# Performance work log

Measured on AMD Instinct MI355X. Metric: run time of the kernel, lower is better.

The kernel has to match this reference:

```python
import jax, jax.numpy as jnp
import numpy as np

EPSILON = 1e-05
LOG_2PI = float(np.log(2.0 * np.pi))


def setup_inputs() -> dict:
    key = jax.random.key(0)
    k1, k2, k3 = jax.random.split(key, 3)
    B, S, K, N = 64, 1000, 12, 80  # batch, seq, n_states, n_channels
    x = jax.random.normal(k1, (B, S, N), dtype=jnp.float32)
    mu = jax.random.normal(k2, (B, K, N), dtype=jnp.float32)
    # Positive-definite covariances per (batch, state)
    A = jax.random.normal(k3, (B, K, N, N), dtype=jnp.float32)
    sigma = A @ jnp.swapaxes(A, -1, -2) / N + jnp.eye(N, dtype=jnp.float32)
    return {"x": x, "mu": mu, "sigma": sigma}


def reference(x, mu, sigma):
    """Batched-over-states MVN log-likelihood.

    x: (B, S, N); mu: (B, K, N); sigma: (B, K, N, N).
    Returns log_likelihood: (B, S, K).
    """
    N = x.shape[-1]
    # add_epsilon with diag=True: epsilon * I on the diagonal
    sigma = sigma + jnp.asarray(EPSILON, sigma.dtype) * jnp.eye(N, dtype=sigma.dtype)
    L = jnp.linalg.cholesky(sigma)  # (B, K, N, N), batched across states
    diff = x[:, :, None, :] - mu[:, None, :, :]  # (B, S, K, N)
    # Solve L z = diff, batched: L -> (B, 1, K, N, N), diff -> (B, S, K, N, 1)
    z = jax.scipy.linalg.solve_triangular(L[:, None], diff[..., None], lower=True)[..., 0]
    quad = jnp.sum(z * z, axis=-1)  # (B, S, K)
    logdet_half = jnp.sum(jnp.log(jnp.diagonal(L, axis1=-2, axis2=-1)), axis=-1)  # (B, K)
    ll = -0.5 * quad - logdet_half[:, None, :] - 0.5 * N * jnp.asarray(LOG_2PI, x.dtype)
    return ll  # (B, S, K)
```

## Files before the change

### kernel.cpp

```cpp
#include <hip/hip_runtime.h>

#define Bb 64
#define Ss 1000
#define Kk 12
#define Nn 80
#define CTERM 73.51508265637381f
#define STA 84

typedef __attribute__((ext_vector_type(8))) short short8;
typedef __attribute__((ext_vector_type(4))) float f32x4;

static __device__ __forceinline__ unsigned short f2bf(float f) {
    unsigned u = __builtin_bit_cast(unsigned, f);
    unsigned r = u + 0x7FFFu + ((u >> 16) & 1u);
    return (unsigned short)(r >> 16);
}
static __device__ __forceinline__ float bf2f(unsigned short h) {
    unsigned u = ((unsigned)h) << 16;
    return __builtin_bit_cast(float, u);
}

__global__ __launch_bounds__(512, 6) void prep_kernel(
    const float* __restrict__ sigma, const float* __restrict__ mu,
    const float* __restrict__ x,
    uint4* __restrict__ wsWh, uint4* __restrict__ wsWl,
    float* __restrict__ wsV, float* __restrict__ wsL,
    uint4* __restrict__ Xh, uint4* __restrict__ Xl, int doX)
{
    __shared__ float Ls[Nn * STA];
    __shared__ float invd[Nn];
    __shared__ float mus[Nn];
    __shared__ float ldp[8];
    __shared__ float vps[8 * Nn];

    const int bk  = blockIdx.x;
    const int tid = threadIdx.x;
    const int w   = tid >> 6;
    const int l   = tid & 63;
    const int r2  = l + 64;

    const float4* sp4 = (const float4*)(sigma + (size_t)bk * Nn * Nn);
    #pragma unroll
    for (int it = 0; it < 4; ++it) {
        int ci = tid + 512 * it;
        if (ci < 1600) {
            int r = ci / 20, c4 = 4 * (ci - 20 * r);
            if (c4 <= r + 3) {
                float4 v = sp4[ci];
                *(float4*)&Ls[r * STA + c4] = v;
            }
        }
    }
    if (tid < Nn) mus[tid] = mu[(size_t)bk * Nn + tid];
    __syncthreads();
    if (tid < Nn) Ls[tid * STA + tid] += 1e-5f;
    __syncthreads();

    float ldacc = 0.0f;
    for (int p = 0; p < 20; ++p) {
        const int j0 = 4 * p;
        const bool a1 = (l >= j0);
        const bool a2 = (l < 16) && (r2 >= j0);

        if (w == (p & 7)) {
            float B00 = Ls[j0*STA+j0];
            float B10 = Ls[(j0+1)*STA+j0], B11 = Ls[(j0+1)*STA+j0+1];
            float B20 = Ls[(j0+2)*STA+j0], B21 = Ls[(j0+2)*STA+j0+1], B22 = Ls[(j0+2)*STA+j0+2];
            float B30 = Ls[(j0+3)*STA+j0], B31 = Ls[(j0+3)*STA+j0+1], B32 = Ls[(j0+3)*STA+j0+2], B33 = Ls[(j0+3)*STA+j0+3];
            float rv0 = rsqrtf(B00);
            float l10 = B10*rv0, l20 = B20*rv0, l30 = B30*rv0;
            float t11 = fmaf(-l10,l10,B11);                    float rv1 = rsqrtf(t11);
            float l21 = fmaf(-l20,l10,B21)*rv1;
            float l31 = fmaf(-l30,l10,B31)*rv1;
            float t22 = fmaf(-l21,l21,fmaf(-l20,l20,B22));     float rv2 = rsqrtf(t22);
            float l32 = fmaf(-l31,l21,fmaf(-l30,l20,B32))*rv2;
            float t33 = fmaf(-l32,l32,fmaf(-l31,l31,fmaf(-l30,l30,B33)));
            float rv3 = rsqrtf(t33);
            ldacc += 0.5f * (logf(B00) + logf(t11) + logf(t22) + logf(t33));
            if (l == 0) { invd[j0]=rv0; invd[j0+1]=rv1; invd[j0+2]=rv2; invd[j0+3]=rv3; }

            if (a1) {
                float4 a = *(float4*)&Ls[l * STA + j0];
                float b0 = a.x * rv0;
                float b1 = fmaf(-l10, b0, a.y) * rv1;
                float b2 = fmaf(-l21, b1, fmaf(-l20, b0, a.z)) * rv2;
                float b3 = fmaf(-l32, b2, fmaf(-l31, b1, fmaf(-l30, b0, a.w))) * rv3;
                *(float4*)&Ls[l * STA + j0] = make_float4(b0, b1, b2, b3);
            }
            if (a2) {
                float4 a = *(float4*)&Ls[r2 * STA + j0];
                float c0 = a.x * rv0;
                float c1 = fmaf(-l10, c0, a.y) * rv1;
                float c2 = fmaf(-l21, c1, fmaf(-l20, c0, a.z)) * rv2;
                float c3 = fmaf(-l32, c2, fmaf(-l31, c1, fmaf(-l30, c0, a.w))) * rv3;
                *(float4*)&Ls[r2 * STA + j0] = make_float4(c0, c1, c2, c3);
            }
        }
        __syncthreads();

        const int gs0 = p + 1;
        const int g0 = gs0 + ((w - gs0) & 7);
        #pragma unroll 2
        for (int g = g0; g < 20; g += 8) {
            const int cb = 4 * g;
            float4 q0 = *(const float4*)&Ls[(cb+0) * STA + j0];
            float4 q1 = *(const float4*)&Ls[(cb+1) * STA + j0];
            float4 q2 = *(const float4*)&Ls[(cb+2) * STA + j0];
            float4 q3 = *(const float4*)&Ls[(cb+3) * STA + j0];
            {
                const int R = cb + l;
                if (R < Nn) {
                    float4 pv = *(const float4*)&Ls[R * STA + j0];
                    float4 t  = *(float4*)&Ls[R * STA + cb];
                    t.x = fmaf(-pv.x,q0.x, fmaf(-pv.y,q0.y, fmaf(-pv.z,q0.z, fmaf(-pv.w,q0.w, t.x))));
                    t.y = fmaf(-pv.x,q1.x, fmaf(-pv.y,q1.y, fmaf(-pv.z,q1.z, fmaf(-pv.w,q1.w, t.y))));
                    t.z = fmaf(-pv.x,q2.x, fmaf(-pv.y,q2.y, fmaf(-pv.z,q2.z, fmaf(-pv.w,q2.w, t.z))));
                    t.w = fmaf(-pv.x,q3.x, fmaf(-pv.y,q3.y, fmaf(-pv.z,q3.z, fmaf(-pv.w,q3.w, t.w))));
                    *(float4*)&Ls[R * STA + cb] = t;
                }
            }
            if (cb + 64 < Nn) {
                const int R = cb + 64 + l;
                if (R < Nn) {
                    float4 pv = *(const float4*)&Ls[R * STA + j0];
                    float4 t  = *(float4*)&Ls[R * STA + cb];
                    t.x = fmaf(-pv.x,q0.x, fmaf(-pv.y,q0.y, fmaf(-pv.z,q0.z, fmaf(-pv.w,q0.w, t.x))));
                    t.y = fmaf(-pv.x,q1.x, fmaf(-pv.y,q1.y, fmaf(-pv.z,q1.z, fmaf(-pv.w,q1.w, t.y))));
                    t.z = fmaf(-pv.x,q2.x, fmaf(-pv.y,q2.y, fmaf(-pv.z,q2.z, fmaf(-pv.w,q2.w, t.z))));
                    t.w = fmaf(-pv.x,q3.x, fmaf(-pv.y,q3.y, fmaf(-pv.z,q3.z, fmaf(-pv.w,q3.w, t.w))));
                    *(float4*)&Ls[R * STA + cb] = t;
                }
            }
        }
    }
    if (l == 0) ldp[w] = ldacc;
    __syncthreads();
    if (tid == 0) wsL[bk] = ldp[0]+ldp[1]+ldp[2]+ldp[3]+ldp[4]+ldp[5]+ldp[6]+ldp[7];

    for (int i = tid; i < Nn * Nn; i += 512) {
        int r = i / Nn, c = i - Nn * r;
        if (c > r) Ls[r * STA + c] = 0.0f;
    }
    __syncthreads();

    for (int p = 0; p < 20; ++p) {
        const int i0 = 4 * p;
        const bool b1a = (i0 + 3 >= l);
        const bool b2a = (l < 16) && (i0 + 3 >= r2);

        if (w == (p & 7)) {
            float m10 = Ls[(i0+1)*STA + i0];
            float m20 = Ls[(i0+2)*STA + i0];
            float m30 = Ls[(i0+3)*STA + i0];
            float m21 = Ls[(i0+2)*STA + i0+1];
            float m31 = Ls[(i0+3)*STA + i0+1];
            float m32 = Ls[(i0+3)*STA + i0+2];
            float4 iv = *(const float4*)&invd[i0];
            if (b1a) {
                float4 a = *(float4*)&Ls[l * STA + i0];
                if (l >= i0)
                    a = make_float4(l==i0?1.f:0.f, l==i0+1?1.f:0.f, l==i0+2?1.f:0.f, l==i0+3?1.f:0.f);
                float w0 = a.x * iv.x;
                float w1 = fmaf(-w0, m10, a.y) * iv.y;
                float w2 = fmaf(-w1, m21, fmaf(-w0, m20, a.z)) * iv.z;
                float w3 = fmaf(-w2, m32, fmaf(-w1, m31, fmaf(-w0, m30, a.w))) * iv.w;
                *(float4*)&Ls[l * STA + i0] = make_float4(w0, w1, w2, w3);
            }
            if (b2a) {
                float4 a = *(float4*)&Ls[r2 * STA + i0];
                if (r2 >= i0)
                    a = make_float4(r2==i0?1.f:0.f, r2==i0+1?1.f:0.f, r2==i0+2?1.f:0.f, r2==i0+3?1.f:0.f);
                float v0 = a.x * iv.x;
                float v1 = fmaf(-v0, m10, a.y) * iv.y;
                float v2 = fmaf(-v1, m21, fmaf(-v0, m20, a.z)) * iv.z;
                float v3 = fmaf(-v2, m32, fmaf(-v1, m31, fmaf(-v0, m30, a.w))) * iv.w;
                *(float4*)&Ls[r2 * STA + i0] = make_float4(v0, v1, v2, v3);
            }
        }
        __syncthreads();

        float4 wv = make_float4(0.f,0.f,0.f,0.f), vv = make_float4(0.f,0.f,0.f,0.f);
        if (b1a) wv = *(float4*)&Ls[l * STA + i0];
        if (b2a) vv = *(float4*)&Ls[r2 * STA + i0];
        if (b1a | b2a) {
            const int gs0 = p + 1;
            const int g0 = gs0 + ((w - gs0) & 7);
            for (int g = g0; g < 20; g += 8) {
                float4 q0 = *(const float4*)&Ls[(4*g+0) * STA + i0];
                float4 q1 = *(const float4*)&Ls[(4*g+1) * STA + i0];
                float4 q2 = *(const float4*)&Ls[(4*g+2) * STA + i0];
                float4 q3 = *(const float4*)&Ls[(4*g+3) * STA + i0];
                if (b1a) {
                    float4 t = *(float4*)&Ls[l * STA + 4*g];
                    t.x = fmaf(-wv.x,q0.x, fmaf(-wv.y,q0.y, fmaf(-wv.z,q0.z, fmaf(-wv.w,q0.w, t.x))));
                    t.y = fmaf(-wv.x,q1.x, fmaf(-wv.y,q1.y, fmaf(-wv.z,q1.z, fmaf(-wv.w,q1.w, t.y))));
                    t.z = fmaf(-wv.x,q2.x, fmaf(-wv.y,q2.y, fmaf(-wv.z,q2.z, fmaf(-wv.w,q2.w, t.z))));
                    t.w = fmaf(-wv.x,q3.x, fmaf(-wv.y,q3.y, fmaf(-wv.z,q3.z, fmaf(-wv.w,q3.w, t.w))));
                    *(float4*)&Ls[l * STA + 4*g] = t;
                }
                if (b2a) {
                    float4 t = *(float4*)&Ls[r2 * STA + 4*g];
                    t.x = fmaf(-vv.x,q0.x, fmaf(-vv.y,q0.y, fmaf(-vv.z,q0.z, fmaf(-vv.w,q0.w, t.x))));
                    t.y = fmaf(-vv.x,q1.x, fmaf(-vv.y,q1.y, fmaf(-vv.z,q1.z, fmaf(-vv.w,q1.w, t.y))));
                    t.z = fmaf(-vv.x,q2.x, fmaf(-vv.y,q2.y, fmaf(-vv.z,q2.z, fmaf(-vv.w,q2.w, t.z))));
                    t.w = fmaf(-vv.x,q3.x, fmaf(-vv.y,q3.y, fmaf(-vv.z,q3.z, fmaf(-vv.w,q3.w, t.w))));
                    *(float4*)&Ls[r2 * STA + 4*g] = t;
                }
            }
        }
    }
    __syncthreads();

    {
        float s1 = 0.f, s2 = 0.f;
        const int c0 = 10 * w;
        #pragma unroll 2
        for (int cc = 0; cc < 10; ++cc) {
            int c = c0 + cc;
            float mc = mus[c];
            float e1 = (c <= l)  ? Ls[c * STA + l]  : 0.f;
            s1 = fmaf(e1, mc, s1);
            if (l < 16) {
                float e2 = (c <= r2) ? Ls[c * STA + r2] : 0.f;
                s2 = fmaf(e2, mc, s2);
            }
        }
        vps[w * Nn + l] = s1;
        if (l < 16) vps[w * Nn + r2] = s2;
        __syncthreads();
        if (tid < Nn) {
            float acc = 0.f;
            #pragma unroll
            for (int ww = 0; ww < 8; ++ww) acc += vps[ww * Nn + tid];
            wsV[(size_t)bk * Nn + tid] = acc;
        }
    }

    const int n = l & 15, quad = l >> 4;
    uint4* ph = wsWh + (size_t)bk * 800;
    uint4* pq = wsWl + (size_t)bk * 800;
    for (int f = w; f < 10; f += 8) {
        int ks = f / 5, mt = f - 5 * ks;
        int m = 16 * mt + n, kb = 32 * ks + 8 * quad;
        unsigned hh[8], lo[8];
        #pragma unroll
        for (int j = 0; j < 8; ++j) {
            float wj = (m >= kb + j) ? Ls[(kb + j) * STA + m] : 0.f;
            unsigned short h = f2bf(wj);
            hh[j] = h; lo[j] = f2bf(wj - bf2f(h));
        }
        ph[f*64 + l] = make_uint4(hh[0]|(hh[1]<<16), hh[2]|(hh[3]<<16), hh[4]|(hh[5]<<16), hh[6]|(hh[7]<<16));
        pq[f*64 + l] = make_uint4(lo[0]|(lo[1]<<16), lo[2]|(lo[3]<<16), lo[4]|(lo[5]<<16), lo[6]|(lo[7]<<16));
    }
    if (w < 5) {
        int mt = w;
        if (quad < 2) {
            int m = 16 * mt + n, kb = 64 + 8 * quad;
            unsigned hh[8], lo[8];
            #pragma unroll
            for (int j = 0; j < 8; ++j) {
                float wj = (m >= kb + j) ? Ls[(kb + j) * STA + m] : 0.f;
                unsigned short h = f2bf(wj);
                hh[j] = h; lo[j] = f2bf(wj - bf2f(h));
            }
            ph[640 + mt*32 + l] = make_uint4(hh[0]|(hh[1]<<16), hh[2]|(hh[3]<<16), hh[4]|(hh[5]<<16), hh[6]|(hh[7]<<16));
            pq[640 + mt*32 + l] = make_uint4(lo[0]|(lo[1]<<16), lo[2]|(lo[3]<<16), lo[4]|(lo[5]<<16), lo[6]|(lo[7]<<16));
        }
    }

    if (doX) {
        const int wid = bk * 8 + w;
        const int qd = l >> 4, n2 = l & 15;
        #pragma unroll
        for (int it = 0; it < 2; ++it) {
            int G = wid + 6144 * it;
            if (G >= 12096) break;
            int b2  = G / 189;
            int rem = G - b2 * 189;
            int sg  = rem / 3, ks = rem - 3 * sg;
            int s   = sg * 16 + n2;
            int k0  = 32 * ks + 8 * qd;
            float d[8] = {0.f,0.f,0.f,0.f,0.f,0.f,0.f,0.f};
            if (s < Ss) {
                const float* xp = x + ((size_t)b2 * Ss + s) * Nn + k0;
                float4 f0 = *(const float4*)xp;
                float4 f1 = *(const float4*)(xp + 4);
                d[0]=f0.x; d[1]=f0.y; d[2]=f0.z; d[3]=f0.w;
                d[4]=f1.x; d[5]=f1.y; d[6]=f1.z; d[7]=f1.w;
            }
            unsigned hh[8], lo[8];
            #pragma unroll
            for (int j = 0; j < 8; ++j) {
                unsigned short h = f2bf(d[j]);
                hh[j] = h; lo[j] = f2bf(d[j] - bf2f(h));
            }
            size_t slot = ((size_t)(b2 * 64 + sg) * 3 + ks) * 64 + l;
            Xh[slot] = make_uint4(hh[0]|(hh[1]<<16), hh[2]|(hh[3]<<16), hh[4]|(hh[5]<<16), hh[6]|(hh[7]<<16));
            Xl[slot] = make_uint4(lo[0]|(lo[1]<<16), lo[2]|(lo[3]<<16), lo[4]|(lo[5]<<16), lo[6]|(lo[7]<<16));
        }
    }
}

__global__ __launch_bounds__(256) void ll_kernel2(
    const uint4* __restrict__ Xh, const uint4* __restrict__ Xl,
    const uint4* __restrict__ wsWh, const uint4* __restrict__ wsWl,
    const float* __restrict__ wsV, const float* __restrict__ wsL,
    float* __restrict__ out)
{
    __shared__ uint4 WhL[960], WlL[960];
    const int b = blockIdx.x;
    const int k = blockIdx.y;
    const int bk = b * Kk + k;
    const int tid = threadIdx.x;
    const int wv = tid >> 6, lane = tid & 63;
    const int n = lane & 15, quad = lane >> 4;

    const uint4* gh = wsWh + (size_t)bk * 800;
    const uint4* gl = wsWl + (size_t)bk * 800;
    #pragma unroll
    for (int it = 0; it < 3; ++it) {
        int i = tid + 256 * it;
        if (i < 640) { WhL[i] = gh[i]; WlL[i] = gl[i]; }
    }
    #pragma unroll
    for (int it = 0; it < 2; ++it) {
        int i = tid + 256 * it;
        if (i < 320) {
            int mt = i >> 6, ln = i & 63, qd = (ln >> 4);
            uint4 vh = make_uint4(0,0,0,0), vl = make_uint4(0,0,0,0);
            if (qd < 2) { vh = gh[640 + mt*32 + ln]; vl = gl[640 + mt*32 + ln]; }
            WhL[640 + i] = vh; WlL[640 + i] = vl;
        }
    }
    __syncthreads();

    const float ld = wsL[bk];
    f32x4 vf[5];
    #pragma unroll
    for (int mt = 0; mt < 5; ++mt)
        vf[mt] = *(const f32x4*)&wsV[(size_t)bk * Nn + 16*mt + 4*quad];

    for (int st = 0; st < 8; ++st) {
        const int sg0 = st * 8 + wv * 2;
        short8 bh[2][3], bl[2][3];
        #pragma unroll
        for (int t = 0; t < 2; ++t)
            #pragma unroll
            for (int ks = 0; ks < 3; ++ks) {
                size_t base = ((size_t)(b * 64 + sg0 + t) * 3 + ks) * 64 + lane;
                bh[t][ks] = __builtin_bit_cast(short8, Xh[base]);
                bl[t][ks] = __builtin_bit_cast(short8, Xl[base]);
            }

        f32x4 acc[2][5];
        #pragma unroll
        for (int t = 0; t < 2; ++t)
            #pragma unroll
            for (int mt = 0; mt < 5; ++mt) acc[t][mt] = (f32x4){0.f,0.f,0.f,0.f};

        #pragma unroll
        for (int ks = 0; ks < 3; ++ks) {
            #pragma unroll
            for (int mt = 0; mt < 5; ++mt) {
                const int fi = (ks < 2) ? (ks*5 + mt)*64 + lane : 640 + mt*64 + lane;
                short8 wh = __builtin_bit_cast(short8, WhL[fi]);
                short8 wl = __builtin_bit_cast(short8, WlL[fi]);
                #pragma unroll
                for (int t = 0; t < 2; ++t) {
                    acc[t][mt] = __builtin_amdgcn_mfma_f32_16x16x32_bf16(wh, bh[t][ks], acc[t][mt], 0, 0, 0);
                    acc[t][mt] = __builtin_amdgcn_mfma_f32_16x16x32_bf16(wl, bh[t][ks], acc[t][mt], 0, 0, 0);
                    acc[t][mt] = __builtin_amdgcn_mfma_f32_16x16x32_bf16(wh, bl[t][ks], acc[t][mt], 0, 0, 0);
                }
            }
        }

        #pragma unroll
        for (int t = 0; t < 2; ++t) {
            float q2 = 0.f;
            #pragma unroll
            for (int mt = 0; mt < 5; ++mt)
                #pragma unroll
                for (int r = 0; r < 4; ++r) {
                    float y = acc[t][mt][r] - vf[mt][r];
                    q2 = fmaf(y, y, q2);
                }
            q2 += __shfl_xor(q2, 16, 64);
            q2 += __shfl_xor(q2, 32, 64);
            int gs = st * 128 + wv * 32 + 16 * t + n;
            if (lane < 16 && gs < Ss)
                out[((size_t)b * Ss + gs) * Kk + k] = -0.5f * q2 - ld - CTERM;
        }
    }
}

__global__ __launch_bounds__(256) void ll_kernel(
    const float* __restrict__ x,
    const uint4* __restrict__ wsWh, const uint4* __restrict__ wsWl,
    const float* __restrict__ wsV, const float* __restrict__ wsL,
    float* __restrict__ out)
{
    const int b    = blockIdx.x;
    const int st   = blockIdx.y;
    const int tid  = threadIdx.x;
    const int wv   = tid >> 6, lane = tid & 63;
    const int n    = lane & 15, quad = lane >> 4;
    const int sbase = st * 128 + wv * 32;

    short8 xh[2][3], xl[2][3];
    #pragma unroll
    for (int t = 0; t < 2; ++t) {
        int gs = sbase + 16 * t + n;
        #pragma unroll
        for (int ks = 0; ks < 3; ++ks) {
            int kb = 32 * ks + 8 * quad;
            float d[8] = {0.f,0.f,0.f,0.f,0.f,0.f,0.f,0.f};
            if (gs < Ss && kb < Nn) {
                const float* xp = x + ((size_t)b * Ss + gs) * Nn + kb;
                float4 f0 = *(const float4*)xp;
                float4 f1 = *(const float4*)(xp + 4);
                d[0]=f0.x; d[1]=f0.y; d[2]=f0.z; d[3]=f0.w;
                d[4]=f1.x; d[5]=f1.y; d[6]=f1.z; d[7]=f1.w;
            }
            short8 h, lo2;
            #pragma unroll
            for (int j = 0; j < 8; ++j) {
                unsigned short hv = f2bf(d[j]);
                h[j]   = (short)hv;
                lo2[j] = (short)f2bf(d[j] - bf2f(hv));
            }
            xh[t][ks] = h; xl[t][ks] = lo2;
        }
    }

    for (int k = 0; k < Kk; ++k) {
        const int bk = b * Kk + k;
        const uint4* ah_p = wsWh + (size_t)bk * 800;
        const uint4* al_p = wsWl + (size_t)bk * 800;

        f32x4 acc[2][5];
        #pragma unroll
        for (int t = 0; t < 2; ++t)
            #pragma unroll
            for (int mt = 0; mt < 5; ++mt) acc[t][mt] = (f32x4){0.f,0.f,0.f,0.f};

        #pragma unroll
        for (int ks = 0; ks < 3; ++ks) {
            short8 ah[5], al[5];
            if (ks < 2) {
                #pragma unroll
                for (int mt = 0; mt < 5; ++mt) {
                    ah[mt] = __builtin_bit_cast(short8, ah_p[(ks*5 + mt)*64 + lane]);
                    al[mt] = __builtin_bit_cast(short8, al_p[(ks*5 + mt)*64 + lane]);
                }
            } else {
                #pragma unroll
                for (int mt = 0; mt < 5; ++mt) {
                    uint4 zh = make_uint4(0,0,0,0), zl = make_uint4(0,0,0,0);
                    if (quad < 2) {
                        zh = ah_p[640 + mt*32 + lane];
                        zl = al_p[640 + mt*32 + lane];
                    }
                    ah[mt] = __builtin_bit_cast(short8, zh);
                    al[mt] = __builtin_bit_cast(short8, zl);
                }
            }
            #pragma unroll
            for (int mt = 0; mt < 5; ++mt)
                #pragma unroll
                for (int t = 0; t < 2; ++t) {
                    acc[t][mt] = __builtin_amdgcn_mfma_f32_16x16x32_bf16(ah[mt], xh[t][ks], acc[t][mt], 0, 0, 0);
                    acc[t][mt] = __builtin_amdgcn_mfma_f32_16x16x32_bf16(al[mt], xh[t][ks], acc[t][mt], 0, 0, 0);
                    acc[t][mt] = __builtin_amdgcn_mfma_f32_16x16x32_bf16(ah[mt], xl[t][ks], acc[t][mt], 0, 0, 0);
                }
        }

        float ld = wsL[bk];
        f32x4 vf[5];
        #pragma unroll
        for (int mt = 0; mt < 5; ++mt)
            vf[mt] = *(const f32x4*)&wsV[(size_t)bk * Nn + 16*mt + 4*quad];
        #pragma unroll
        for (int t = 0; t < 2; ++t) {
            float q2 = 0.f;
            #pragma unroll
            for (int mt = 0; mt < 5; ++mt)
                #pragma unroll
                for (int r = 0; r < 4; ++r) {
                    float y = acc[t][mt][r] - vf[mt][r];
                    q2 = fmaf(y, y, q2);
                }
            q2 += __shfl_xor(q2, 16, 64);
            q2 += __shfl_xor(q2, 32, 64);
            int gs = sbase + 16 * t + n;
            if (lane < 16 && gs < Ss)
                out[((size_t)b * Ss + gs) * Kk + k] = -0.5f * q2 - ld - CTERM;
        }
    }
}

#define ST1 81
__global__ __launch_bounds__(256) void mvn_ll_fallback(
    const float* __restrict__ x, const float* __restrict__ mu,
    const float* __restrict__ sigma, float* __restrict__ out)
{
    __shared__ float Ls[Nn * ST1];
    __shared__ float invd[Nn];
    __shared__ float mus[Nn];
    __shared__ float logdet_s;

    const int bk = blockIdx.x, b = bk / Kk, k = bk - b * Kk;
    const int tid = threadIdx.x, nt = blockDim.x;

    const float* sp = sigma + (size_t)bk * Nn * Nn;
    for (int t = tid; t < Nn * Nn; t += nt) Ls[(t / Nn) * ST1 + (t % Nn)] = sp[t];
    if (tid < Nn) mus[tid] = mu[(size_t)bk * Nn + tid];
    __syncthreads();
    if (tid < Nn) Ls[tid * ST1 + tid] += 1e-5f;
    __syncthreads();
    for (int j = 0; j < Nn; ++j) {
        if (tid == 0) {
            float d = sqrtf(Ls[j * ST1 + j]);
            Ls[j * ST1 + j] = d; invd[j] = 1.0f / d;
        }
        __syncthreads();
        const float inv = invd[j];
        for (int i = j + 1 + tid; i < Nn; i += nt) Ls[i * ST1 + j] *= inv;
        __syncthreads();
        for (int t = tid; t < Nn * Nn; t += nt) {
            int r = t / Nn, c = t % Nn;
            if (r > j && c > j && c <= r)
                Ls[r * ST1 + c] -= Ls[r * ST1 + j] * Ls[c * ST1 + j];
        }
        __syncthreads();
    }
    if (tid == 0) {
        float a = 0.f; for (int j = 0; j < Nn; ++j) a += logf(Ls[j * ST1 + j]);
        logdet_s = a;
    }
    __syncthreads();
    const float ld = logdet_s;
    for (int s = tid; s < Ss; s += nt) {
        const float4* xp = (const float4*)(x + ((size_t)b * Ss + s) * Nn);
        float a[Nn];
        #pragma unroll
        for (int q = 0; q < Nn / 4; ++q) {
            float4 v = xp[q];
            a[4*q+0] = v.x - mus[4*q+0]; a[4*q+1] = v.y - mus[4*q+1];
            a[4*q+2] = v.z - mus[4*q+2]; a[4*q+3] = v.w - mus[4*q+3];
        }
        #pragma unroll
        for (int i = 0; i < Nn; ++i) {
            float t = a[i];
            #pragma unroll
            for (int j = 0; j < i; ++j) t = fmaf(-Ls[i * ST1 + j], a[j], t);
            a[i] = t * invd[i];
        }
        float quad = 0.f;
        #pragma unroll
        for (int i = 0; i < Nn; ++i) quad = fmaf(a[i], a[i], quad);
        out[((size_t)b * Ss + s) * Kk + k] = -0.5f * quad - ld - CTERM;
    }
}

extern "C" void kernel_launch(void* const* d_in, const int* in_sizes, int n_in,
                              void* d_out, int out_size, void* d_ws, size_t ws_size,
                              hipStream_t stream) {
    const float* x     = (const float*)d_in[0];
    const float* mu    = (const float*)d_in[1];
    const float* sigma = (const float*)d_in[2];
    float* out = (float*)d_out;

    const size_t nBK   = (size_t)Bb * Kk;
    const size_t nWu4  = nBK * 800;
    const size_t nXu4  = (size_t)Bb * 64 * 3 * 64;
    const size_t need_mid  = nWu4 * 16 * 2 + nBK * Nn * 4 + nBK * 4;
    const size_t need_full = need_mid + nXu4 * 16 * 2;

    if (ws_size >= need_full) {
        uint4* wsWh = (uint4*)d_ws;
        uint4* wsWl = wsWh + nWu4;
        uint4* Xh   = wsWl + nWu4;
        uint4* Xl   = Xh + nXu4;
        float* wsV  = (float*)(Xl + nXu4);
        float* wsL  = wsV + nBK * Nn;
        prep_kernel<<<dim3(Bb * Kk), dim3(512), 0, stream>>>(
            sigma, mu, x, wsWh, wsWl, wsV, wsL, Xh, Xl, 1);
        ll_kernel2<<<dim3(Bb, Kk), dim3(256), 0, stream>>>(Xh, Xl, wsWh, wsWl, wsV, wsL, out);
    } else if (ws_size >= need_mid) {
        uint4* wsWh = (uint4*)d_ws;
        uint4* wsWl = wsWh + nWu4;
        float* wsV  = (float*)(wsWl + nWu4);
        float* wsL  = wsV + nBK * Nn;
        prep_kernel<<<dim3(Bb * Kk), dim3(512), 0, stream>>>(
            sigma, mu, x, wsWh, wsWl, wsV, wsL, (uint4*)nullptr, (uint4*)nullptr, 0);
        ll_kernel<<<dim3(Bb, 8), dim3(256), 0, stream>>>(x, wsWh, wsWl, wsV, wsL, out);
    } else {
        mvn_ll_fallback<<<dim3(Bb * Kk), dim3(256), 0, stream>>>(x, mu, sigma, out);
    }
}
```

Before: 161.6 us.

## Fuse Cholesky prep and MFMA log-likelihood into a single kernel

Merges the Cholesky/bf16-split prep kernel and the MFMA quadratic-form kernel into one kernel with one block per (batch, state). The split weights, mu-projection and log-determinant stay in shared memory instead of going through a workspace, and each block converts x to bf16 hi/lo itself. This removes a kernel launch, the workspace round trip and the separate pre-conversion of x. In exchange, x is reconverted 12 times per batch (once per state), shared memory grows with the extra weight arrays, and the fallback paths are deleted.

After: 335.4 us. 108% more time.

```diff
diff --git a/kernel.cpp b/kernel.cpp
--- a/kernel.cpp
+++ b/kernel.cpp
@@ -20,20 +20,21 @@
     return __builtin_bit_cast(float, u);
 }
 
-__global__ __launch_bounds__(512, 6) void prep_kernel(
+__global__ __launch_bounds__(512, 6) void fused_ll_kernel(
     const float* __restrict__ sigma, const float* __restrict__ mu,
-    const float* __restrict__ x,
-    uint4* __restrict__ wsWh, uint4* __restrict__ wsWl,
-    float* __restrict__ wsV, float* __restrict__ wsL,
-    uint4* __restrict__ Xh, uint4* __restrict__ Xl, int doX)
+    const float* __restrict__ x, float* __restrict__ out)
 {
     __shared__ float Ls[Nn * STA];
+    __shared__ uint4 WhL[800], WlL[800];
     __shared__ float invd[Nn];
     __shared__ float mus[Nn];
+    __shared__ float vls[Nn];
     __shared__ float ldp[8];
-    __shared__ float vps[8 * Nn];
-
-    const int bk  = blockIdx.x;
+    __shared__ float lds_ld;
+
+    const int b   = blockIdx.x;
+    const int k   = blockIdx.y;
+    const int bk  = b * Kk + k;
     const int tid = threadIdx.x;
     const int w   = tid >> 6;
     const int l   = tid & 63;
@@ -135,7 +136,7 @@
     }
     if (l == 0) ldp[w] = ldacc;
     __syncthreads();
-    if (tid == 0) wsL[bk] = ldp[0]+ldp[1]+ldp[2]+ldp[3]+ldp[4]+ldp[5]+ldp[6]+ldp[7];
+    if (tid == 0) lds_ld = ldp[0]+ldp[1]+ldp[2]+ldp[3]+ldp[4]+ldp[5]+ldp[6]+ldp[7];
 
     for (int i = tid; i < Nn * Nn; i += 512) {
         int r = i / Nn, c = i - Nn * r;
@@ -212,6 +213,7 @@
     __syncthreads();
 
     {
+        float* vps = (float*)WhL;
         float s1 = 0.f, s2 = 0.f;
         const int c0 = 10 * w;
         #pragma unroll 2
@@ -232,13 +234,12 @@
             float acc = 0.f;
             #pragma unroll
             for (int ww = 0; ww < 8; ++ww) acc += vps[ww * Nn + tid];
-            wsV[(size_t)bk * Nn + tid] = acc;
-        }
+            vls[tid] = acc;
+        }
+        __syncthreads();
     }
 
     const int n = l & 15, quad = l >> 4;
-    uint4* ph = wsWh + (size_t)bk * 800;
-    uint4* pq = wsWl + (size_t)bk * 800;
     for (int f = w; f < 10; f += 8) {
         int ks = f / 5, mt = f - 5 * ks;
         int m = 16 * mt + n, kb = 32 * ks + 8 * quad;
@@ -249,8 +250,8 @@
             unsigned short h = f2bf(wj);
             hh[j] = h; lo[j] = f2bf(wj - bf2f(h));
         }
-        ph[f*64 + l] = make_uint4(hh[0]|(hh[1]<<16), hh[2]|(hh[3]<<16), hh[4]|(hh[5]<<16), hh[6]|(hh[7]<<16));
-        pq[f*64 + l] = make_uint4(lo[0]|(lo[1]<<16), lo[2]|(lo[3]<<16), lo[4]|(lo[5]<<16), lo[6]|(lo[7]<<16));
+        WhL[f*64 + l] = make_uint4(hh[0]|(hh[1]<<16), hh[2]|(hh[3]<<16), hh[4]|(hh[5]<<16), hh[6]|(hh[7]<<16));
+        WlL[f*64 + l] = make_uint4(lo[0]|(lo[1]<<16), lo[2]|(lo[3]<<16), lo[4]|(lo[5]<<16), lo[6]|(lo[7]<<16));
     }
     if (w < 5) {
         int mt = w;
@@ -263,153 +264,18 @@
                 unsigned short h = f2bf(wj);
                 hh[j] = h; lo[j] = f2bf(wj - bf2f(h));
             }
-            ph[640 + mt*32 + l] = make_uint4(hh[0]|(hh[1]<<16), hh[2]|(hh[3]<<16), hh[4]|(hh[5]<<16), hh[6]|(hh[7]<<16));
-            pq[640 + mt*32 + l] = make_uint4(lo[0]|(lo[1]<<16), lo[2]|(lo[3]<<16), lo[4]|(lo[5]<<16), lo[6]|(lo[7]<<16));
-        }
-    }
-
-    if (doX) {
-        const int wid = bk * 8 + w;
-        const int qd = l >> 4, n2 = l & 15;
-        #pragma unroll
-        for (int it = 0; it < 2; ++it) {
-            int G = wid + 6144 * it;
-            if (G >= 12096) break;
-            int b2  = G / 189;
-            int rem = G - b2 * 189;
-            int sg  = rem / 3, ks = rem - 3 * sg;
-            int s   = sg * 16 + n2;
-            int k0  = 32 * ks + 8 * qd;
-            float d[8] = {0.f,0.f,0.f,0.f,0.f,0.f,0.f,0.f};
-            if (s < Ss) {
-                const float* xp = x + ((size_t)b2 * Ss + s) * Nn + k0;
-                float4 f0 = *(const float4*)xp;
-                float4 f1 = *(const float4*)(xp + 4);
-                d[0]=f0.x; d[1]=f0.y; d[2]=f0.z; d[3]=f0.w;
-                d[4]=f1.x; d[5]=f1.y; d[6]=f1.z; d[7]=f1.w;
-            }
-            unsigned hh[8], lo[8];
-            #pragma unroll
-            for (int j = 0; j < 8; ++j) {
-                unsigned short h = f2bf(d[j]);
-                hh[j] = h; lo[j] = f2bf(d[j] - bf2f(h));
-            }
-            size_t slot = ((size_t)(b2 * 64 + sg) * 3 + ks) * 64 + l;
-            Xh[slot] = make_uint4(hh[0]|(hh[1]<<16), hh[2]|(hh[3]<<16), hh[4]|(hh[5]<<16), hh[6]|(hh[7]<<16));
-            Xl[slot] = make_uint4(lo[0]|(lo[1]<<16), lo[2]|(lo[3]<<16), lo[4]|(lo[5]<<16), lo[6]|(lo[7]<<16));
-        }
-    }
-}
-
-__global__ __launch_bounds__(256) void ll_kernel2(
-    const uint4* __restrict__ Xh, const uint4* __restrict__ Xl,
-    const uint4* __restrict__ wsWh, const uint4* __restrict__ wsWl,
-    const float* __restrict__ wsV, const float* __restrict__ wsL,
-    float* __restrict__ out)
-{
-    __shared__ uint4 WhL[960], WlL[960];
-    const int b = blockIdx.x;
-    const int k = blockIdx.y;
-    const int bk = b * Kk + k;
-    const int tid = threadIdx.x;
-    const int wv = tid >> 6, lane = tid & 63;
-    const int n = lane & 15, quad = lane >> 4;
-
-    const uint4* gh = wsWh + (size_t)bk * 800;
-    const uint4* gl = wsWl + (size_t)bk * 800;
-    #pragma unroll
-    for (int it = 0; it < 3; ++it) {
-        int i = tid + 256 * it;
-        if (i < 640) { WhL[i] = gh[i]; WlL[i] = gl[i]; }
-    }
-    #pragma unroll
-    for (int it = 0; it < 2; ++it) {
-        int i = tid + 256 * it;
-        if (i < 320) {
-            int mt = i >> 6, ln = i & 63, qd = (ln >> 4);
-            uint4 vh = make_uint4(0,0,0,0), vl = make_uint4(0,0,0,0);
-            if (qd < 2) { vh = gh[640 + mt*32 + ln]; vl = gl[640 + mt*32 + ln]; }
-            WhL[640 + i] = vh; WlL[640 + i] = vl;
-        }
-    }
-    __syncthreads();
-
-    const float ld = wsL[bk];
-    f32x4 vf[5];
-    #pragma unroll
-    for (int mt = 0; mt < 5; ++mt)
-        vf[mt] = *(const f32x4*)&wsV[(size_t)bk * Nn + 16*mt + 4*quad];
-
-    for (int st = 0; st < 8; ++st) {
-        const int sg0 = st * 8 + wv * 2;
-        short8 bh[2][3], bl[2][3];
-        #pragma unroll
-        for (int t = 0; t < 2; ++t)
-            #pragma unroll
-            for (int ks = 0; ks < 3; ++ks) {
-                size_t base = ((size_t)(b * 64 + sg0 + t) * 3 + ks) * 64 + lane;
-                bh[t][ks] = __builtin_bit_cast(short8, Xh[base]);
-                bl[t][ks] = __builtin_bit_cast(short8, Xl[base]);
-            }
-
-        f32x4 acc[2][5];
-        #pragma unroll
-        for (int t = 0; t < 2; ++t)
-            #pragma unroll
-            for (int mt = 0; mt < 5; ++mt) acc[t][mt] = (f32x4){0.f,0.f,0.f,0.f};
-
-        #pragma unroll
-        for (int ks = 0; ks < 3; ++ks) {
-            #pragma unroll
-            for (int mt = 0; mt < 5; ++mt) {
-                const int fi = (ks < 2) ? (ks*5 + mt)*64 + lane : 640 + mt*64 + lane;
-                short8 wh = __builtin_bit_cast(short8, WhL[fi]);
-                short8 wl = __builtin_bit_cast(short8, WlL[fi]);
-                #pragma unroll
-                for (int t = 0; t < 2; ++t) {
-                    acc[t][mt] = __builtin_amdgcn_mfma_f32_16x16x32_bf16(wh, bh[t][ks], acc[t][mt], 0, 0, 0);
-                    acc[t][mt] = __builtin_amdgcn_mfma_f32_16x16x32_bf16(wl, bh[t][ks], acc[t][mt], 0, 0, 0);
-                    acc[t][mt] = __builtin_amdgcn_mfma_f32_16x16x32_bf16(wh, bl[t][ks], acc[t][mt], 0, 0, 0);
-                }
-            }
-        }
-
-        #pragma unroll
-        for (int t = 0; t < 2; ++t) {
-            float q2 = 0.f;
-            #pragma unroll
-            for (int mt = 0; mt < 5; ++mt)
-                #pragma unroll
-                for (int r = 0; r < 4; ++r) {
-                    float y = acc[t][mt][r] - vf[mt][r];
-                    q2 = fmaf(y, y, q2);
-                }
-            q2 += __shfl_xor(q2, 16, 64);
-            q2 += __shfl_xor(q2, 32, 64);
-            int gs = st * 128 + wv * 32 + 16 * t + n;
-            if (lane < 16 && gs < Ss)
-                out[((size_t)b * Ss + gs) * Kk + k] = -0.5f * q2 - ld - CTERM;
-        }
-    }
-}
-
-__global__ __launch_bounds__(256) void ll_kernel(
-    const float* __restrict__ x,
-    const uint4* __restrict__ wsWh, const uint4* __restrict__ wsWl,
-    const float* __restrict__ wsV, const float* __restrict__ wsL,
-    float* __restrict__ out)
-{
-    const int b    = blockIdx.x;
-    const int st   = blockIdx.y;
-    const int tid  = threadIdx.x;
-    const int wv   = tid >> 6, lane = tid & 63;
-    const int n    = lane & 15, quad = lane >> 4;
-    const int sbase = st * 128 + wv * 32;
-
-    short8 xh[2][3], xl[2][3];
-    #pragma unroll
-    for (int t = 0; t < 2; ++t) {
-        int gs = sbase + 16 * t + n;
+            WhL[640 + mt*32 + l] = make_uint4(hh[0]|(hh[1]<<16), hh[2]|(hh[3]<<16), hh[4]|(hh[5]<<16), hh[6]|(hh[7]<<16));
+            WlL[640 + mt*32 + l] = make_uint4(lo[0]|(lo[1]<<16), lo[2]|(lo[3]<<16), lo[4]|(lo[5]<<16), lo[6]|(lo[7]<<16));
+        }
+    }
+    __syncthreads();
+
+    const float ld = lds_ld;
+    for (int it = 0; it < 8; ++it) {
+        const int sg = it * 8 + w;
+        const int gs = sg * 16 + n;
+
+        short8 bh[3], bl[3];
         #pragma unroll
         for (int ks = 0; ks < 3; ++ks) {
             int kb = 32 * ks + 8 * quad;
@@ -428,137 +294,50 @@
                 h[j]   = (short)hv;
                 lo2[j] = (short)f2bf(d[j] - bf2f(hv));
             }
-            xh[t][ks] = h; xl[t][ks] = lo2;
-        }
-    }
-
-    for (int k = 0; k < Kk; ++k) {
-        const int bk = b * Kk + k;
-        const uint4* ah_p = wsWh + (size_t)bk * 800;
-        const uint4* al_p = wsWl + (size_t)bk * 800;
-
-        f32x4 acc[2][5];
-        #pragma unroll
-        for (int t = 0; t < 2; ++t)
-            #pragma unroll
-            for (int mt = 0; mt < 5; ++mt) acc[t][mt] = (f32x4){0.f,0.f,0.f,0.f};
+            bh[ks] = h; bl[ks] = lo2;
+        }
+
+        f32x4 acc[5];
+        #pragma unroll
+        for (int mt = 0; mt < 5; ++mt) acc[mt] = (f32x4){0.f,0.f,0.f,0.f};
 
         #pragma unroll
         for (int ks = 0; ks < 3; ++ks) {
-            short8 ah[5], al[5];
-            if (ks < 2) {
-                #pragma unroll
-                for (int mt = 0; mt < 5; ++mt) {
-                    ah[mt] = __builtin_bit_cast(short8, ah_p[(ks*5 + mt)*64 + lane]);
-                    al[mt] = __builtin_bit_cast(short8, al_p[(ks*5 + mt)*64 + lane]);
-                }
-            } else {
-                #pragma unroll
-                for (int mt = 0; mt < 5; ++mt) {
+            #pragma unroll
+            for (int mt = 0; mt < 5; ++mt) {
+                short8 wh, wl;
+                if (ks < 2) {
+                    wh = __builtin_bit_cast(short8, WhL[(ks*5 + mt)*64 + l]);
+                    wl = __builtin_bit_cast(short8, WlL[(ks*5 + mt)*64 + l]);
+                } else {
                     uint4 zh = make_uint4(0,0,0,0), zl = make_uint4(0,0,0,0);
                     if (quad < 2) {
-                        zh = ah_p[640 + mt*32 + lane];
-                        zl = al_p[640 + mt*32 + lane];
+                        zh = WhL[640 + mt*32 + l];
+                        zl = WlL[640 + mt*32 + l];
                     }
-                    ah[mt] = __builtin_bit_cast(short8, zh);
-                    al[mt] = __builtin_bit_cast(short8, zl);
-                }
-            }
-            #pragma unroll
-            for (int mt = 0; mt < 5; ++mt)
-                #pragma unroll
-                for (int t = 0; t < 2; ++t) {
-                    acc[t][mt] = __builtin_amdgcn_mfma_f32_16x16x32_bf16(ah[mt], xh[t][ks], acc[t][mt], 0, 0, 0);
-                    acc[t][mt] = __builtin_amdgcn_mfma_f32_16x16x32_bf16(al[mt], xh[t][ks], acc[t][mt], 0, 0, 0);
-                    acc[t][mt] = __builtin_amdgcn_mfma_f32_16x16x32_bf16(ah[mt], xl[t][ks], acc[t][mt], 0, 0, 0);
-                }
-        }
-
-        float ld = wsL[bk];
-        f32x4 vf[5];
-        #pragma unroll
-        for (int mt = 0; mt < 5; ++mt)
-            vf[mt] = *(const f32x4*)&wsV[(size_t)bk * Nn + 16*mt + 4*quad];
-        #pragma unroll
-        for (int t = 0; t < 2; ++t) {
-            float q2 = 0.f;
-            #pragma unroll
-            for (int mt = 0; mt < 5; ++mt)
-                #pragma unroll
-                for (int r = 0; r < 4; ++r) {
-                    float y = acc[t][mt][r] - vf[mt][r];
-                    q2 = fmaf(y, y, q2);
-                }
-            q2 += __shfl_xor(q2, 16, 64);
-            q2 += __shfl_xor(q2, 32, 64);
-            int gs = sbase + 16 * t + n;
-            if (lane < 16 && gs < Ss)
-                out[((size_t)b * Ss + gs) * Kk + k] = -0.5f * q2 - ld - CTERM;
-        }
-    }
-}
-
-#define ST1 81
-__global__ __launch_bounds__(256) void mvn_ll_fallback(
-    const float* __restrict__ x, const float* __restrict__ mu,
-    const float* __restrict__ sigma, float* __restrict__ out)
-{
-    __shared__ float Ls[Nn * ST1];
-    __shared__ float invd[Nn];
-    __shared__ float mus[Nn];
-    __shared__ float logdet_s;
-
-    const int bk = blockIdx.x, b = bk / Kk, k = bk - b * Kk;
-    const int tid = threadIdx.x, nt = blockDim.x;
-
-    const float* sp = sigma + (size_t)bk * Nn * Nn;
-    for (int t = tid; t < Nn * Nn; t += nt) Ls[(t / Nn) * ST1 + (t % Nn)] = sp[t];
-    if (tid < Nn) mus[tid] = mu[(size_t)bk * Nn + tid];
-    __syncthreads();
-    if (tid < Nn) Ls[tid * ST1 + tid] += 1e-5f;
-    __syncthreads();
-    for (int j = 0; j < Nn; ++j) {
-        if (tid == 0) {
-            float d = sqrtf(Ls[j * ST1 + j]);
-            Ls[j * ST1 + j] = d; invd[j] = 1.0f / d;
-        }
-        __syncthreads();
-        const float inv = invd[j];
-        for (int i = j + 1 + tid; i < Nn; i += nt) Ls[i * ST1 + j] *= inv;
-        __syncthreads();
-        for (int t = tid; t < Nn * Nn; t += nt) {
-            int r = t / Nn, c = t % Nn;
-            if (r > j && c > j && c <= r)
-                Ls[r * ST1 + c] -= Ls[r * ST1 + j] * Ls[c * ST1 + j];
-        }
-        __syncthreads();
-    }
-    if (tid == 0) {
-        float a = 0.f; for (int j = 0; j < Nn; ++j) a += logf(Ls[j * ST1 + j]);
-        logdet_s = a;
-    }
-    __syncthreads();
-    const float ld = logdet_s;
-    for (int s = tid; s < Ss; s += nt) {
-        const float4* xp = (const float4*)(x + ((size_t)b * Ss + s) * Nn);
-        float a[Nn];
-        #pragma unroll
-        for (int q = 0; q < Nn / 4; ++q) {
-            float4 v = xp[q];
-            a[4*q+0] = v.x - mus[4*q+0]; a[4*q+1] = v.y - mus[4*q+1];
-            a[4*q+2] = v.z - mus[4*q+2]; a[4*q+3] = v.w - mus[4*q+3];
-        }
-        #pragma unroll
-        for (int i = 0; i < Nn; ++i) {
-            float t = a[i];
-            #pragma unroll
-            for (int j = 0; j < i; ++j) t = fmaf(-Ls[i * ST1 + j], a[j], t);
-            a[i] = t * invd[i];
-        }
-        float quad = 0.f;
-        #pragma unroll
-        for (int i = 0; i < Nn; ++i) quad = fmaf(a[i], a[i], quad);
-        out[((size_t)b * Ss + s) * Kk + k] = -0.5f * quad - ld - CTERM;
+                    wh = __builtin_bit_cast(short8, zh);
+                    wl = __builtin_bit_cast(short8, zl);
+                }
+                acc[mt] = __builtin_amdgcn_mfma_f32_16x16x32_bf16(wh, bh[ks], acc[mt], 0, 0, 0);
+                acc[mt] = __builtin_amdgcn_mfma_f32_16x16x32_bf16(wl, bh[ks], acc[mt], 0, 0, 0);
+                acc[mt] = __builtin_amdgcn_mfma_f32_16x16x32_bf16(wh, bl[ks], acc[mt], 0, 0, 0);
+            }
+        }
+
+        float q2 = 0.f;
+        #pragma unroll
+        for (int mt = 0; mt < 5; ++mt) {
+            f32x4 vfm = *(const f32x4*)&vls[16*mt + 4*quad];
+            #pragma unroll
+            for (int r = 0; r < 4; ++r) {
+                float y = acc[mt][r] - vfm[r];
+                q2 = fmaf(y, y, q2);
+            }
+        }
+        q2 += __shfl_xor(q2, 16, 64);
+        q2 += __shfl_xor(q2, 32, 64);
+        if (l < 16 && gs < Ss)
+            out[((size_t)b * Ss + gs) * Kk + k] = -0.5f * q2 - ld - CTERM;
     }
 }
 
@@ -569,32 +348,7 @@
     const float* mu    = (const float*)d_in[1];
     const float* sigma = (const float*)d_in[2];
     float* out = (float*)d_out;
-
-    const size_t nBK   = (size_t)Bb * Kk;
-    const size_t nWu4  = nBK * 800;
-    const size_t nXu4  = (size_t)Bb * 64 * 3 * 64;
-    const size_t need_mid  = nWu4 * 16 * 2 + nBK * Nn * 4 + nBK * 4;
-    const size_t need_full = need_mid + nXu4 * 16 * 2;
-
-    if (ws_size >= need_full) {
-        uint4* wsWh = (uint4*)d_ws;
-        uint4* wsWl = wsWh + nWu4;
-        uint4* Xh   = wsWl + nWu4;
-        uint4* Xl   = Xh + nXu4;
-        float* wsV  = (float*)(Xl + nXu4);
-        float* wsL  = wsV + nBK * Nn;
-        prep_kernel<<<dim3(Bb * Kk), dim3(512), 0, stream>>>(
-            sigma, mu, x, wsWh, wsWl, wsV, wsL, Xh, Xl, 1);
-        ll_kernel2<<<dim3(Bb, Kk), dim3(256), 0, stream>>>(Xh, Xl, wsWh, wsWl, wsV, wsL, out);
-    } else if (ws_size >= need_mid) {
-        uint4* wsWh = (uint4*)d_ws;
-        uint4* wsWl = wsWh + nWu4;
-        float* wsV  = (float*)(wsWl + nWu4);
-        float* wsL  = wsV + nBK * Nn;
-        prep_kernel<<<dim3(Bb * Kk), dim3(512), 0, stream>>>(
-            sigma, mu, x, wsWh, wsWl, wsV, wsL, (uint4*)nullptr, (uint4*)nullptr, 0);
-        ll_kernel<<<dim3(Bb, 8), dim3(256), 0, stream>>>(x, wsWh, wsWl, wsV, wsL, out);
-    } else {
-        mvn_ll_fallback<<<dim3(Bb * Kk), dim3(256), 0, stream>>>(x, mu, sigma, out);
-    }
+    (void)d_ws; (void)ws_size;
+
+    fused_ll_kernel<<<dim3(Bb, Kk), dim3(512), 0, stream>>>(sigma, mu, x, out);
 }
```
